# Performance work log

Hardware: AMD Instinct MI355X
Metric: run time of the kernel (lower is better)

## Reference

```python
import jax, jax.numpy as jnp
import numpy as np

NEG_SLOPE = 0.2

def gat_conv(x, edge, W, att_src, att_dst, bias, heads, out_ch, concat):
    # x: [N, F_in], edge: [2, E] (self-loops already included)
    N = x.shape[0]
    src, dst = edge[0], edge[1]
    h = (x @ W).reshape(N, heads, out_ch)                     # [N, H, C]
    a_src = jnp.sum(h * att_src, axis=-1)                     # [N, H]
    a_dst = jnp.sum(h * att_dst, axis=-1)                     # [N, H]
    e = jax.nn.leaky_relu(a_src[src] + a_dst[dst], NEG_SLOPE)  # [E, H]
    # segment softmax over incoming edges of each dst node
    e_max = jax.ops.segment_max(e, dst, num_segments=N)       # [N, H]
    e_exp = jnp.exp(e - e_max[dst])                           # [E, H]
    denom = jax.ops.segment_sum(e_exp, dst, num_segments=N)   # [N, H]
    alpha = e_exp / denom[dst]                                # [E, H]
    msg = h[src] * alpha[:, :, None]                          # [E, H, C]
    out = jax.ops.segment_sum(msg, dst, num_segments=N)       # [N, H, C]
    if concat:
        out = out.reshape(N, heads * out_ch)
    else:
        out = out.mean(axis=1)
    return out + bias


def setup_inputs() -> dict:
    key = jax.random.key(0)
    ks = jax.random.split(key, 10)
    N, E = 50000, 1600000
    F_in, H, C1, n_cls = 256, 4, 64, 40
    x = jax.random.normal(ks[0], (N, F_in), dtype=jnp.float32)
    edge_index = jax.random.randint(ks[1], (2, E), 0, N, dtype=jnp.int64)
    s1 = 1.0 / np.sqrt(F_in)
    s2 = 1.0 / np.sqrt(H * C1)
    return {
        "x": x,
        "edge_index": edge_index,
        "W1": jax.random.normal(ks[2], (F_in, H * C1), dtype=jnp.float32) * s1,
        "att_src1": jax.random.normal(ks[3], (H, C1), dtype=jnp.float32) * s2,
        "att_dst1": jax.random.normal(ks[4], (H, C1), dtype=jnp.float32) * s2,
        "b1": jnp.zeros((H * C1,), dtype=jnp.float32),
        "W2": jax.random.normal(ks[5], (H * C1, n_cls), dtype=jnp.float32) * s2,
        "att_src2": jax.random.normal(ks[6], (1, n_cls), dtype=jnp.float32) * 0.1,
        "att_dst2": jax.random.normal(ks[7], (1, n_cls), dtype=jnp.float32) * 0.1,
        "b2": jnp.zeros((n_cls,), dtype=jnp.float32),
    }


def reference(x, edge_index, W1, att_src1, att_dst1, b1, W2, att_src2, att_dst2, b2):
    N = x.shape[0]
    # PyG GATConv adds self-loops by default
    loops = jnp.arange(N, dtype=edge_index.dtype)
    edge = jnp.concatenate([edge_index, jnp.stack([loops, loops])], axis=1)
    # dropout is identity in eval mode
    h = gat_conv(x, edge, W1, att_src1, att_dst1, b1, heads=4, out_ch=64, concat=True)
    h = jax.nn.elu(h)
    out = gat_conv(h, edge, W2, att_src2, att_dst2, b2, heads=1, out_ch=40, concat=False)
    return out
```

## Files before the change

### kernel.cpp

```cpp
#include <hip/hip_runtime.h>
#include <hip/hip_bf16.h>

typedef short bf16x8 __attribute__((ext_vector_type(8)));
typedef float f32x4 __attribute__((ext_vector_type(4)));
typedef float f32x2 __attribute__((ext_vector_type(2)));
typedef unsigned short u16x8 __attribute__((ext_vector_type(8)));

#define CHUNK 4096
#define BCAP 16384

__device__ __forceinline__ float wred_sum(float v) {
  #pragma unroll
  for (int off = 32; off > 0; off >>= 1)
    v += __shfl_xor(v, off, 64);
  return v;
}
__device__ __forceinline__ float b2f(unsigned short u) {
  union { unsigned int i; float f; } x;
  x.i = ((unsigned int)u) << 16;
  return x.f;
}
__device__ __forceinline__ unsigned short f2bu(float f) {
  __hip_bfloat16 b = __float2bfloat16(f);
  return *(unsigned short*)&b;
}
__device__ __forceinline__ void pkfma(f32x2& acc, f32x2 v, f32x2 w) {
  asm volatile("v_pk_fma_f32 %0, %1, %2, %0" : "+v"(acc) : "v"(v), "v"(w));
}
__device__ __forceinline__ void qfma(f32x2* acc2, unsigned int u, f32x2 wp) {
  f32x2 a, b;
  a[0] = (float)(u & 0xFFu);         a[1] = (float)((u >> 8) & 0xFFu);
  b[0] = (float)((u >> 16) & 0xFFu); b[1] = (float)(u >> 24);
  pkfma(acc2[0], a, wp);
  pkfma(acc2[1], b, wp);
}
__device__ __forceinline__ void bffma(f32x2& acc, unsigned int up, f32x2 wp) {
  union { unsigned int i; float f; } lo, hi;
  lo.i = up << 16; hi.i = up & 0xFFFF0000u;
  f32x2 v; v[0] = lo.f; v[1] = hi.f;
  pkfma(acc, v, wp);
}
__device__ __forceinline__ float ldf(const void* p, long long i, int is16) {
  return is16 ? __bfloat162float(((const __hip_bfloat16*)p)[i])
              : ((const float*)p)[i];
}
__device__ __forceinline__ int edge_at(const int* e, long long idx, int is64) {
  return is64 ? (int)((const long long*)e)[idx] : e[idx];
}

__global__ void detect_kernel(const int* __restrict__ edge, int n_edge_check,
                              const unsigned int* __restrict__ xw, int n_x_check,
                              int* __restrict__ flag,
                              int* __restrict__ bcursor, int NB) {
  __shared__ int s_nz, s_cnt, s_tot;
  int tid = threadIdx.x;
  for (int b = tid; b < NB; b += 256) bcursor[b] = b * BCAP;
  if (tid == 0) { s_nz = 0; s_cnt = 0; s_tot = 0; }
  __syncthreads();
  int nz = 0;
  for (int k = tid; k < n_edge_check; k += 256)
    if (edge[2 * k + 1] != 0) nz = 1;
  if (nz) atomicOr(&s_nz, 1);
  int c = 0, t = 0;
  for (int k = tid; k < n_x_check; k += 256) {
    unsigned int w = xw[k];
    if (w == 0u) continue;
    t++;
    unsigned int e = (w >> 7) & 0xFFu;
    if (e >= 100u && e <= 150u) c++;
  }
  atomicAdd(&s_cnt, c);
  atomicAdd(&s_tot, t);
  __syncthreads();
  if (tid == 0) {
    flag[0] = (s_nz == 0) ? 1 : 0;
    flag[1] = (s_cnt * 10 > s_tot * 6) ? 1 : 0;
  }
}

__global__ __launch_bounds__(256) void partition_kernel(
    const int* __restrict__ edge, int E, int N, const int* __restrict__ flag,
    int* __restrict__ bcursor, unsigned int* __restrict__ part, int NB) {
  __shared__ int cnt[1024];
  __shared__ int loff[1025];
  __shared__ int gpos[1024];
  __shared__ int lcur[1024];
  __shared__ unsigned int staged[CHUNK];
  __shared__ int staged_addr[CHUNK];
  __shared__ int s[256];
  __shared__ int rbase;
  int tid = threadIdx.x;
  long long base = (long long)blockIdx.x * CHUNK;
  long long total = (long long)E + N;
  int maxa = NB * BCAP - 1;
  int here = (int)min((long long)CHUNK, total - base);
  for (int b = tid; b < NB; b += 256) cnt[b] = 0;
  if (tid == 0) rbase = 0;
  __syncthreads();
  int is64 = flag[0];
  int myb[16];
  unsigned int myp[16];
  #pragma unroll
  for (int j = 0; j < 16; j++) {
    long long i = base + j * 256 + tid;
    myb[j] = -1;
    if (i < total) {
      int d, sv;
      if (i < E) {
        sv = edge_at(edge, i, is64);
        d = edge_at(edge, (long long)E + i, is64);
      } else {
        sv = d = (int)(i - E);
      }
      d = min(max(d, 0), N - 1);
      sv = min(max(sv, 0), N - 1);
      myb[j] = d >> 8;
      myp[j] = ((unsigned int)(d & 255) << 24) | (unsigned int)sv;
      atomicAdd(&cnt[myb[j]], 1);
    }
  }
  __syncthreads();
  for (int c0 = 0; c0 < NB; c0 += 256) {
    int idx = c0 + tid;
    int v = (idx < NB) ? cnt[idx] : 0;
    s[tid] = v;
    __syncthreads();
    for (int off = 1; off < 256; off <<= 1) {
      int t = (tid >= off) ? s[tid - off] : 0;
      __syncthreads();
      s[tid] += t;
      __syncthreads();
    }
    int mb = rbase;
    if (idx < NB) loff[idx] = mb + s[tid] - v;
    __syncthreads();
    if (tid == 0) rbase = mb + s[255];
    __syncthreads();
  }
  __syncthreads();
  for (int b = tid; b < NB; b += 256) {
    int c = cnt[b];
    gpos[b] = c ? atomicAdd(&bcursor[b], c) : 0;
    lcur[b] = loff[b];
  }
  __syncthreads();
  #pragma unroll
  for (int j = 0; j < 16; j++) {
    if (myb[j] >= 0) {
      int b = myb[j];
      int slot = atomicAdd(&lcur[b], 1);
      staged[slot] = myp[j];
      staged_addr[slot] = min(gpos[b] + (slot - loff[b]), maxa);
    }
  }
  __syncthreads();
  for (int i = tid; i < here; i += 256)
    part[staged_addr[i]] = staged[i];
}

__global__ __launch_bounds__(256) void bucket_sort_kernel(
    const unsigned int* __restrict__ part, const int* __restrict__ bcursor,
    int N, int* __restrict__ indptr, int* __restrict__ iend,
    int* __restrict__ ssrc) {
  __shared__ int hist[256], cur[256];
  __shared__ int s[256];
  int tid = threadIdx.x;
  int b = blockIdx.x;
  int begin = b * BCAP, end = bcursor[b];
  hist[tid] = 0;
  __syncthreads();
  for (int i = begin + tid; i < end; i += 256)
    atomicAdd(&hist[part[i] >> 24], 1);
  __syncthreads();
  int v = hist[tid];
  s[tid] = v;
  __syncthreads();
  for (int off = 1; off < 256; off <<= 1) {
    int t = (tid >= off) ? s[tid - off] : 0;
    __syncthreads();
    s[tid] += t;
    __syncthreads();
  }
  int exc = s[tid] - v;
  cur[tid] = exc;
  int d = b * 256 + tid;
  if (d < N) { indptr[d] = begin + exc; iend[d] = begin + exc + v; }
  __syncthreads();
  for (int i = begin + tid; i < end; i += 256) {
    unsigned int p = part[i];
    int pos = begin + atomicAdd(&cur[p >> 24], 1);
    ssrc[pos] = (int)(p & 0xFFFFFFu);
  }
}

__global__ void prep_kernel(const void* __restrict__ x, __hip_bfloat16* __restrict__ xb,
                            long long n_valid4, long long nconv4,
                            const void* __restrict__ W1v, const void* __restrict__ W2v,
                            __hip_bfloat16* __restrict__ Wt1, __hip_bfloat16* __restrict__ Wt2,
                            int F, int HC, int C2, int C2p,
                            const int* __restrict__ dflag) {
  int f16 = dflag[1];
  long long i = blockIdx.x * 256LL + threadIdx.x;
  if (i < nconv4) {
    ushort4 o;
    if (i < n_valid4) {
      if (f16) {
        o = ((const ushort4*)x)[i];
      } else {
        float4 v = ((const float4*)x)[i];
        o.x = f2bu(v.x); o.y = f2bu(v.y); o.z = f2bu(v.z); o.w = f2bu(v.w);
      }
    } else {
      o.x = o.y = o.z = o.w = 0;
    }
    ((ushort4*)xb)[i] = o;
    return;
  }
  long long j = i - nconv4;
  int n1 = HC * F;
  if (j < n1) {
    int idx = (int)j;
    int n = idx / F, k = idx - n * F;
    Wt1[idx] = __float2bfloat16(ldf(W1v, (long long)k * HC + n, f16));
  } else {
    int jj = (int)(j - n1);
    if (jj >= C2p * HC) return;
    int n = jj / HC, k = jj - n * HC;
    float v = (n < C2) ? ldf(W2v, (long long)k * C2 + n, f16) : 0.f;
    Wt2[jj] = __float2bfloat16(v);
  }
}

__global__ __launch_bounds__(256) void mfma_gemm_kernel(
    const __hip_bfloat16* __restrict__ A, const __hip_bfloat16* __restrict__ BtT,
    __hip_bfloat16* __restrict__ Cb,
    const void* __restrict__ attS, const void* __restrict__ attD,
    float* __restrict__ aS, float* __restrict__ aD,
    float2* __restrict__ aSq, int att_stride,
    int M, int Nout, int K, int quant,
    unsigned char* __restrict__ h1q,
    const int* __restrict__ dflag) {
  int f16 = dflag[1];
  int tid = threadIdx.x;
  int w = tid >> 6, l = tid & 63;
  int m_lane = l & 15, q = l >> 4;
  int row0 = blockIdx.x * 64, col0 = blockIdx.y * 64;
  const __hip_bfloat16* Arow = A + (long long)(row0 + w * 16 + m_lane) * K + q * 8;
  const __hip_bfloat16* Brow = BtT + (long long)(col0 + m_lane) * K + q * 8;
  f32x4 acc[4] = {};
  #pragma unroll 4
  for (int k0 = 0; k0 < K; k0 += 32) {
    bf16x8 af = *(const bf16x8*)(Arow + k0);
    #pragma unroll
    for (int t = 0; t < 4; t++) {
      bf16x8 bf = *(const bf16x8*)(Brow + (long long)t * 16 * K + k0);
      acc[t] = __builtin_amdgcn_mfma_f32_16x16x32_bf16(af, bf, acc[t], 0, 0, 0);
    }
  }
  #pragma unroll
  for (int r = 0; r < 4; r++) {
    int gr = row0 + w * 16 + q * 4 + r;
    float ps = 0.f, pd = 0.f, vmax = 0.f;
    #pragma unroll
    for (int t = 0; t < 4; t++) {
      int gc = col0 + t * 16 + m_lane;
      float v = acc[t][r];
      if (gc < Nout) {
        ps += v * ldf(attS, gc, f16);
        pd += v * ldf(attD, gc, f16);
        vmax = fmaxf(vmax, fabsf(v));
        if (!quant && gr < M) Cb[(long long)gr * Nout + gc] = __float2bfloat16(v);
      }
    }
    #pragma unroll
    for (int off = 1; off < 16; off <<= 1) {
      ps += __shfl_xor(ps, off, 64);
      pd += __shfl_xor(pd, off, 64);
      vmax = fmaxf(vmax, __shfl_xor(vmax, off, 64));
    }
    if (quant && gr < M) {
      float qinv = (vmax > 0.f) ? 127.f / vmax : 0.f;
      #pragma unroll
      for (int t = 0; t < 4; t++) {
        int gc = col0 + t * 16 + m_lane;
        h1q[(long long)gr * 256 + gc] =
            (unsigned char)(__float2int_rn(acc[t][r] * qinv) + 128);
      }
      if (m_lane == 0) {
        float2 sq; sq.x = ps; sq.y = vmax * (1.f / 127.f);
        aSq[(long long)gr * att_stride + blockIdx.y] = sq;
      }
    }
    if (m_lane == 0 && gr < M) {
      if (!quant) aS[(long long)gr * att_stride + blockIdx.y] = ps;
      aD[(long long)gr * att_stride + blockIdx.y] = pd;
    }
  }
}

__global__ __launch_bounds__(256) void aggregate1_kernel(
    const int* __restrict__ indptr, const int* __restrict__ iend,
    const int* __restrict__ ssrc,
    const unsigned char* __restrict__ h1q, const float2* __restrict__ a_sq,
    const float* __restrict__ a_dst, const void* __restrict__ b1,
    __hip_bfloat16* __restrict__ h2b, int N, const int* __restrict__ dflag) {
  int f16 = dflag[1];
  int w = threadIdx.x >> 6, l = threadIdx.x & 63;
  int d = blockIdx.x * 4 + w;
  if (d >= N) return;
  int q = l >> 4;
  int e16 = l & 15;
  int hb = (l & 12) << 2;
  int chb = (l & 15) << 4;
  int begin = indptr[d], end = iend[d];
  float adst = a_dst[d * 4 + q];
  int s0 = ssrc[begin];
  float den = 0.f, accS = 0.f;
  f32x2 acc2[8] = {};
  for (int c = begin; c < end; c += 32) {
    int cnt = end - c;
    int sj0 = s0, sj1 = s0;
    float wj0 = 0.f, wj1 = 0.f, ws0 = 0.f, ws1 = 0.f;
    if (e16 < cnt) {
      sj0 = ssrc[c + e16];
      float2 t = a_sq[sj0 * 4 + q];
      float e = t.x + adst;
      e = (e > 0.f) ? e : 0.2f * e;
      wj0 = __expf(e);
      ws0 = wj0 * t.y;
    }
    if (e16 + 16 < cnt) {
      sj1 = ssrc[c + e16 + 16];
      float2 t = a_sq[sj1 * 4 + q];
      float e = t.x + adst;
      e = (e > 0.f) ? e : 0.2f * e;
      wj1 = __expf(e);
      ws1 = wj1 * t.y;
    }
    den += wj0 + wj1;
    int m0 = cnt < 16 ? cnt : 16;
    int m1 = cnt - 16; m1 = m1 < 0 ? 0 : (m1 > 16 ? 16 : m1);
    int j0 = (m0 + 3) >> 2, j1 = (m1 + 3) >> 2;
    #pragma unroll 4
    for (int j = 0; j < j0; j++) {
      int idx = hb + 4 * j + q;
      int s = __shfl(sj0, idx, 64);
      float wt = __shfl(ws0, idx, 64);
      accS += wt;
      f32x2 wp; wp[0] = wt; wp[1] = wt;
      uint4 uv = *(const uint4*)(h1q + (long long)s * 256 + chb);
      qfma(&acc2[0], uv.x, wp);
      qfma(&acc2[2], uv.y, wp);
      qfma(&acc2[4], uv.z, wp);
      qfma(&acc2[6], uv.w, wp);
    }
    #pragma unroll 4
    for (int j = 0; j < j1; j++) {
      int idx = hb + 4 * j + q;
      int s = __shfl(sj1, idx, 64);
      float wt = __shfl(ws1, idx, 64);
      accS += wt;
      f32x2 wp; wp[0] = wt; wp[1] = wt;
      uint4 uv = *(const uint4*)(h1q + (long long)s * 256 + chb);
      qfma(&acc2[0], uv.x, wp);
      qfma(&acc2[2], uv.y, wp);
      qfma(&acc2[4], uv.z, wp);
      qfma(&acc2[6], uv.w, wp);
    }
  }
  float* af = (float*)acc2;
  #pragma unroll
  for (int i = 0; i < 16; i++) {
    af[i] += __shfl_xor(af[i], 16, 64);
    af[i] += __shfl_xor(af[i], 32, 64);
  }
  accS += __shfl_xor(accS, 16, 64);
  accS += __shfl_xor(accS, 32, 64);
  #pragma unroll
  for (int off = 1; off < 16; off <<= 1)
    den += __shfl_xor(den, off, 64);
  float deh = __shfl(den, hb, 64);
  float inv = 1.f / deh;
  if (l < 16) {
    u16x8 o0, o1;
    #pragma unroll
    for (int i = 0; i < 16; i++) {
      float v = (af[i] - 128.f * accS) * inv + ldf(b1, chb + i, f16);
      v = (v > 0.f) ? v : (__expf(v) - 1.f);
      if (i < 8) o0[i] = f2bu(v); else o1[i - 8] = f2bu(v);
    }
    u16x8* dst = (u16x8*)((unsigned short*)h2b + (long long)d * 256 + chb);
    dst[0] = o0;
    dst[1] = o1;
  }
}

__global__ __launch_bounds__(256) void aggregate2_kernel(
    const int* __restrict__ indptr, const int* __restrict__ iend,
    const int* __restrict__ ssrc,
    const __hip_bfloat16* __restrict__ gb, const float* __restrict__ a_src,
    const float* __restrict__ a_dst, const void* __restrict__ b2,
    void* __restrict__ out, int N, int C, const int* __restrict__ dflag) {
  int f16 = dflag[1];
  int w = threadIdx.x >> 6, l = threadIdx.x & 63;
  int d = blockIdx.x * 4 + w;
  if (d >= N) return;
  int begin = indptr[d], end = iend[d];
  float adst = a_dst[d];
  int eg = l / 10;
  int cq = l - eg * 10;
  bool act = (eg < 6);
  int s0 = ssrc[begin];
  float den = 0.f;
  f32x2 acc01 = {0.f, 0.f}, acc23 = {0.f, 0.f};
  for (int c = begin; c < end; c += 64) {
    int cnt = min(64, end - c);
    int sj = s0;
    float wj = 0.f;
    if (l < cnt) {
      sj = ssrc[c + l];
      float e = a_src[sj] + adst;
      e = (e > 0.f) ? e : 0.2f * e;
      wj = __expf(e);
    }
    den += wj;
    int jm = (cnt + 5) / 6;
    #pragma unroll 4
    for (int j = 0; j < jm; j++) {
      int idx = 6 * j + eg;
      int s = __shfl(sj, idx & 63, 64);
      float wt = __shfl(wj, idx & 63, 64);
      if (!act || idx >= cnt) wt = 0.f;
      uint2 gv = *(const uint2*)((const unsigned short*)gb +
                                 (long long)s * C + 4 * cq);
      f32x2 wp; wp[0] = wt; wp[1] = wt;
      bffma(acc01, gv.x, wp);
      bffma(acc23, gv.y, wp);
    }
  }
  den = wred_sum(den);
  float inv = 1.f / den;
  float a0 = acc01[0], a1 = acc01[1], a2 = acc23[0], a3 = acc23[1];
  #pragma unroll
  for (int k = 1; k < 6; k++) {
    int srcl = cq + 10 * k;
    a0 += __shfl(acc01[0], srcl, 64);
    a1 += __shfl(acc01[1], srcl, 64);
    a2 += __shfl(acc23[0], srcl, 64);
    a3 += __shfl(acc23[1], srcl, 64);
  }
  if (l < 10) {
    float v0 = a0 * inv + ldf(b2, 4 * l + 0, f16);
    float v1 = a1 * inv + ldf(b2, 4 * l + 1, f16);
    float v2 = a2 * inv + ldf(b2, 4 * l + 2, f16);
    float v3 = a3 * inv + ldf(b2, 4 * l + 3, f16);
    long long o = (long long)d * C + 4 * l;
    if (f16) {
      ushort4 ov;
      ov.x = f2bu(v0); ov.y = f2bu(v1); ov.z = f2bu(v2); ov.w = f2bu(v3);
      *(ushort4*)((unsigned short*)out + o) = ov;
    } else {
      float4 ov;
      ov.x = v0; ov.y = v1; ov.z = v2; ov.w = v3;
      *(float4*)((float*)out + o) = ov;
    }
  }
}

extern "C" void kernel_launch(void* const* d_in, const int* in_sizes, int n_in,
                              void* d_out, int out_size, void* d_ws, size_t ws_size,
                              hipStream_t stream) {
  const void* x   = d_in[0];
  const int* edge = (const int*)d_in[1];
  const void* W1  = d_in[2];
  const void* as1 = d_in[3];
  const void* ad1 = d_in[4];
  const void* b1  = d_in[5];
  const void* W2  = d_in[6];
  const void* as2 = d_in[7];
  const void* ad2 = d_in[8];
  const void* b2  = d_in[9];

  const int F  = 256;
  const int HC = 256;
  const int N  = in_sizes[0] / F;
  const int E  = in_sizes[1] / 2;
  const int C2 = in_sizes[9];
  const int C2p = 64;
  const int total = E + N;
  const int NB = (N + 255) / 256;
  const int Mpad = ((N + 63) / 64) * 64;

  char* p = (char*)d_ws;
  auto alloc = [&](size_t bytes) -> void* {
    void* r = (void*)p;
    p += (bytes + 255) & ~(size_t)255;
    return r;
  };
  __hip_bfloat16* xb  = (__hip_bfloat16*)alloc((size_t)Mpad * F * 2);
  unsigned char*  h1q = (unsigned char*)alloc((size_t)Mpad * HC);
  __hip_bfloat16* h2b = (__hip_bfloat16*)alloc((size_t)Mpad * HC * 2);
  __hip_bfloat16* gb  = (__hip_bfloat16*)alloc((size_t)Mpad * C2 * 2);
  __hip_bfloat16* Wt1 = (__hip_bfloat16*)alloc((size_t)HC * F * 2);
  __hip_bfloat16* Wt2 = (__hip_bfloat16*)alloc((size_t)C2p * HC * 2);
  float2* a_sq1 = (float2*)alloc((size_t)N * 4 * 8);
  float* a_dst1 = (float*)alloc((size_t)N * 4 * 4);
  float* a_src2 = (float*)alloc((size_t)N * 4);
  float* a_dst2 = (float*)alloc((size_t)N * 4);
  unsigned int* part = (unsigned int*)alloc((size_t)NB * BCAP * 4);
  int* ssrc     = (int*)alloc((size_t)NB * BCAP * 4);
  int* bcursor  = (int*)alloc((size_t)NB * 4);
  int* indptr   = (int*)alloc((size_t)(N + 1) * 4);
  int* iend     = (int*)alloc((size_t)N * 4);
  int* flag     = (int*)alloc(256);

  detect_kernel<<<1, 256, 0, stream>>>(edge, E < 2048 ? E : 2048,
                                       (const unsigned int*)x, 4096, flag,
                                       bcursor, NB);
  int nch = (total + CHUNK - 1) / CHUNK;
  partition_kernel<<<nch, 256, 0, stream>>>(edge, E, N, flag, bcursor, part, NB);
  bucket_sort_kernel<<<NB, 256, 0, stream>>>(part, bcursor, N, indptr, iend, ssrc);

  long long nconv4 = (long long)Mpad * F / 4;
  long long nprep = nconv4 + (long long)HC * F + (long long)C2p * HC;
  prep_kernel<<<(int)((nprep + 255) / 256), 256, 0, stream>>>(
      x, xb, (long long)N * F / 4, nconv4, W1, W2, Wt1, Wt2, F, HC, C2, C2p, flag);

  dim3 g1(Mpad / 64, HC / 64);
  mfma_gemm_kernel<<<g1, 256, 0, stream>>>(xb, Wt1, nullptr,
                                           as1, ad1, nullptr, a_dst1, a_sq1, 4,
                                           N, HC, F, 1, h1q, flag);
  aggregate1_kernel<<<(N + 3) / 4, 256, 0, stream>>>(indptr, iend, ssrc, h1q, a_sq1,
                                                     a_dst1, b1, h2b, N, flag);

  dim3 g2(Mpad / 64, 1);
  mfma_gemm_kernel<<<g2, 256, 0, stream>>>(h2b, Wt2, gb,
                                           as2, ad2, a_src2, a_dst2, nullptr, 1,
                                           N, C2, HC, 0, nullptr, flag);
  aggregate2_kernel<<<(N + 3) / 4, 256, 0, stream>>>(indptr, iend, ssrc, gb, a_src2, a_dst2,
                                                     b2, d_out, N, C2, flag);
}
```

Baseline: 375.8 us.

## Use grid-stride persistent aggregation and widen edge chunks to 48

Both aggregation kernels now launch a fixed 2048-block grid, and each wave loops over destination nodes with a grid stride instead of handling one node per wave. Aggregate1 processes edges in chunks of 48 (three 16-edge groups) with the three gathers interleaved in one loop, which puts more independent loads in flight. The asm volatile on the packed FMA is dropped so the compiler can schedule it more freely. The aim is less block launch overhead and more memory-level parallelism; the cost is a possible load imbalance across waves from the fixed grid and higher register use.

```diff
diff --git a/kernel.cpp b/kernel.cpp
--- a/kernel.cpp
+++ b/kernel.cpp
@@ -25,7 +25,7 @@
   return *(unsigned short*)&b;
 }
 __device__ __forceinline__ void pkfma(f32x2& acc, f32x2 v, f32x2 w) {
-  asm volatile("v_pk_fma_f32 %0, %1, %2, %0" : "+v"(acc) : "v"(v), "v"(w));
+  asm("v_pk_fma_f32 %0, %1, %2, %0" : "+v"(acc) : "v"(v), "v"(w));
 }
 __device__ __forceinline__ void qfma(f32x2* acc2, unsigned int u, f32x2 wp) {
   f32x2 a, b;
@@ -306,92 +306,112 @@
     __hip_bfloat16* __restrict__ h2b, int N, const int* __restrict__ dflag) {
   int f16 = dflag[1];
   int w = threadIdx.x >> 6, l = threadIdx.x & 63;
-  int d = blockIdx.x * 4 + w;
-  if (d >= N) return;
   int q = l >> 4;
   int e16 = l & 15;
   int hb = (l & 12) << 2;
   int chb = (l & 15) << 4;
-  int begin = indptr[d], end = iend[d];
-  float adst = a_dst[d * 4 + q];
-  int s0 = ssrc[begin];
-  float den = 0.f, accS = 0.f;
-  f32x2 acc2[8] = {};
-  for (int c = begin; c < end; c += 32) {
-    int cnt = end - c;
-    int sj0 = s0, sj1 = s0;
-    float wj0 = 0.f, wj1 = 0.f, ws0 = 0.f, ws1 = 0.f;
-    if (e16 < cnt) {
-      sj0 = ssrc[c + e16];
-      float2 t = a_sq[sj0 * 4 + q];
-      float e = t.x + adst;
-      e = (e > 0.f) ? e : 0.2f * e;
-      wj0 = __expf(e);
-      ws0 = wj0 * t.y;
-    }
-    if (e16 + 16 < cnt) {
-      sj1 = ssrc[c + e16 + 16];
-      float2 t = a_sq[sj1 * 4 + q];
-      float e = t.x + adst;
-      e = (e > 0.f) ? e : 0.2f * e;
-      wj1 = __expf(e);
-      ws1 = wj1 * t.y;
-    }
-    den += wj0 + wj1;
-    int m0 = cnt < 16 ? cnt : 16;
-    int m1 = cnt - 16; m1 = m1 < 0 ? 0 : (m1 > 16 ? 16 : m1);
-    int j0 = (m0 + 3) >> 2, j1 = (m1 + 3) >> 2;
-    #pragma unroll 4
-    for (int j = 0; j < j0; j++) {
-      int idx = hb + 4 * j + q;
-      int s = __shfl(sj0, idx, 64);
-      float wt = __shfl(ws0, idx, 64);
-      accS += wt;
-      f32x2 wp; wp[0] = wt; wp[1] = wt;
-      uint4 uv = *(const uint4*)(h1q + (long long)s * 256 + chb);
-      qfma(&acc2[0], uv.x, wp);
-      qfma(&acc2[2], uv.y, wp);
-      qfma(&acc2[4], uv.z, wp);
-      qfma(&acc2[6], uv.w, wp);
-    }
-    #pragma unroll 4
-    for (int j = 0; j < j1; j++) {
-      int idx = hb + 4 * j + q;
-      int s = __shfl(sj1, idx, 64);
-      float wt = __shfl(ws1, idx, 64);
-      accS += wt;
-      f32x2 wp; wp[0] = wt; wp[1] = wt;
-      uint4 uv = *(const uint4*)(h1q + (long long)s * 256 + chb);
-      qfma(&acc2[0], uv.x, wp);
-      qfma(&acc2[2], uv.y, wp);
-      qfma(&acc2[4], uv.z, wp);
-      qfma(&acc2[6], uv.w, wp);
-    }
-  }
-  float* af = (float*)acc2;
-  #pragma unroll
-  for (int i = 0; i < 16; i++) {
-    af[i] += __shfl_xor(af[i], 16, 64);
-    af[i] += __shfl_xor(af[i], 32, 64);
-  }
-  accS += __shfl_xor(accS, 16, 64);
-  accS += __shfl_xor(accS, 32, 64);
-  #pragma unroll
-  for (int off = 1; off < 16; off <<= 1)
-    den += __shfl_xor(den, off, 64);
-  float deh = __shfl(den, hb, 64);
-  float inv = 1.f / deh;
-  if (l < 16) {
-    u16x8 o0, o1;
+  int stride = gridDim.x * 4;
+  for (int d = blockIdx.x * 4 + w; d < N; d += stride) {
+    int begin = indptr[d], end = iend[d];
+    float adst = a_dst[d * 4 + q];
+    int s0 = ssrc[begin];
+    float den = 0.f, accS = 0.f;
+    f32x2 acc2[8] = {};
+    for (int c = begin; c < end; c += 48) {
+      int cnt = end - c;
+      int sj0 = s0, sj1 = s0, sj2 = s0;
+      float ws0 = 0.f, ws1 = 0.f, ws2 = 0.f;
+      if (e16 < cnt) {
+        sj0 = ssrc[c + e16];
+        float2 t = a_sq[sj0 * 4 + q];
+        float e = t.x + adst;
+        e = (e > 0.f) ? e : 0.2f * e;
+        float wj = __expf(e);
+        den += wj; ws0 = wj * t.y;
+      }
+      if (e16 + 16 < cnt) {
+        sj1 = ssrc[c + 16 + e16];
+        float2 t = a_sq[sj1 * 4 + q];
+        float e = t.x + adst;
+        e = (e > 0.f) ? e : 0.2f * e;
+        float wj = __expf(e);
+        den += wj; ws1 = wj * t.y;
+      }
+      if (e16 + 32 < cnt) {
+        sj2 = ssrc[c + 32 + e16];
+        float2 t = a_sq[sj2 * 4 + q];
+        float e = t.x + adst;
+        e = (e > 0.f) ? e : 0.2f * e;
+        float wj = __expf(e);
+        den += wj; ws2 = wj * t.y;
+      }
+      int m0 = cnt < 16 ? cnt : 16;
+      int m1 = cnt - 16; m1 = m1 < 0 ? 0 : (m1 > 16 ? 16 : m1);
+      int m2 = cnt - 32; m2 = m2 < 0 ? 0 : (m2 > 16 ? 16 : m2);
+      int j0 = (m0 + 3) >> 2, j1 = (m1 + 3) >> 2, j2 = (m2 + 3) >> 2;
+      #pragma unroll 4
+      for (int j = 0; j < j0; j++) {
+        int idx = hb + 4 * j + q;
+        {
+          int s = __shfl(sj0, idx, 64);
+          float wt = __shfl(ws0, idx, 64);
+          accS += wt;
+          f32x2 wp; wp[0] = wt; wp[1] = wt;
+          uint4 uv = *(const uint4*)(h1q + (long long)s * 256 + chb);
+          qfma(&acc2[0], uv.x, wp);
+          qfma(&acc2[2], uv.y, wp);
+          qfma(&acc2[4], uv.z, wp);
+          qfma(&acc2[6], uv.w, wp);
+        }
+        if (j < j1) {
+          int s = __shfl(sj1, idx, 64);
+          float wt = __shfl(ws1, idx, 64);
+          accS += wt;
+          f32x2 wp; wp[0] = wt; wp[1] = wt;
+          uint4 uv = *(const uint4*)(h1q + (long long)s * 256 + chb);
+          qfma(&acc2[0], uv.x, wp);
+          qfma(&acc2[2], uv.y, wp);
+          qfma(&acc2[4], uv.z, wp);
+          qfma(&acc2[6], uv.w, wp);
+        }
+        if (j < j2) {
+          int s = __shfl(sj2, idx, 64);
+          float wt = __shfl(ws2, idx, 64);
+          accS += wt;
+          f32x2 wp; wp[0] = wt; wp[1] = wt;
+          uint4 uv = *(const uint4*)(h1q + (long long)s * 256 + chb);
+          qfma(&acc2[0], uv.x, wp);
+          qfma(&acc2[2], uv.y, wp);
+          qfma(&acc2[4], uv.z, wp);
+          qfma(&acc2[6], uv.w, wp);
+        }
+      }
+    }
+    float* af = (float*)acc2;
     #pragma unroll
     for (int i = 0; i < 16; i++) {
-      float v = (af[i] - 128.f * accS) * inv + ldf(b1, chb + i, f16);
-      v = (v > 0.f) ? v : (__expf(v) - 1.f);
-      if (i < 8) o0[i] = f2bu(v); else o1[i - 8] = f2bu(v);
-    }
-    u16x8* dst = (u16x8*)((unsigned short*)h2b + (long long)d * 256 + chb);
-    dst[0] = o0;
-    dst[1] = o1;
+      af[i] += __shfl_xor(af[i], 16, 64);
+      af[i] += __shfl_xor(af[i], 32, 64);
+    }
+    accS += __shfl_xor(accS, 16, 64);
+    accS += __shfl_xor(accS, 32, 64);
+    #pragma unroll
+    for (int off = 1; off < 16; off <<= 1)
+      den += __shfl_xor(den, off, 64);
+    float deh = __shfl(den, hb, 64);
+    float inv = 1.f / deh;
+    if (l < 16) {
+      u16x8 o0, o1;
+      #pragma unroll
+      for (int i = 0; i < 16; i++) {
+        float v = (af[i] - 128.f * accS) * inv + ldf(b1, chb + i, f16);
+        v = (v > 0.f) ? v : (__expf(v) - 1.f);
+        if (i < 8) o0[i] = f2bu(v); else o1[i - 8] = f2bu(v);
+      }
+      u16x8* dst = (u16x8*)((unsigned short*)h2b + (long long)d * 256 + chb);
+      dst[0] = o0;
+      dst[1] = o1;
+    }
   }
 }
 
@@ -403,66 +423,67 @@
     void* __restrict__ out, int N, int C, const int* __restrict__ dflag) {
   int f16 = dflag[1];
   int w = threadIdx.x >> 6, l = threadIdx.x & 63;
-  int d = blockIdx.x * 4 + w;
-  if (d >= N) return;
-  int begin = indptr[d], end = iend[d];
-  float adst = a_dst[d];
   int eg = l / 10;
   int cq = l - eg * 10;
   bool act = (eg < 6);
-  int s0 = ssrc[begin];
-  float den = 0.f;
-  f32x2 acc01 = {0.f, 0.f}, acc23 = {0.f, 0.f};
-  for (int c = begin; c < end; c += 64) {
-    int cnt = min(64, end - c);
-    int sj = s0;
-    float wj = 0.f;
-    if (l < cnt) {
-      sj = ssrc[c + l];
-      float e = a_src[sj] + adst;
-      e = (e > 0.f) ? e : 0.2f * e;
-      wj = __expf(e);
-    }
-    den += wj;
-    int jm = (cnt + 5) / 6;
-    #pragma unroll 4
-    for (int j = 0; j < jm; j++) {
-      int idx = 6 * j + eg;
-      int s = __shfl(sj, idx & 63, 64);
-      float wt = __shfl(wj, idx & 63, 64);
-      if (!act || idx >= cnt) wt = 0.f;
-      uint2 gv = *(const uint2*)((const unsigned short*)gb +
-                                 (long long)s * C + 4 * cq);
-      f32x2 wp; wp[0] = wt; wp[1] = wt;
-      bffma(acc01, gv.x, wp);
-      bffma(acc23, gv.y, wp);
-    }
-  }
-  den = wred_sum(den);
-  float inv = 1.f / den;
-  float a0 = acc01[0], a1 = acc01[1], a2 = acc23[0], a3 = acc23[1];
-  #pragma unroll
-  for (int k = 1; k < 6; k++) {
-    int srcl = cq + 10 * k;
-    a0 += __shfl(acc01[0], srcl, 64);
-    a1 += __shfl(acc01[1], srcl, 64);
-    a2 += __shfl(acc23[0], srcl, 64);
-    a3 += __shfl(acc23[1], srcl, 64);
-  }
-  if (l < 10) {
-    float v0 = a0 * inv + ldf(b2, 4 * l + 0, f16);
-    float v1 = a1 * inv + ldf(b2, 4 * l + 1, f16);
-    float v2 = a2 * inv + ldf(b2, 4 * l + 2, f16);
-    float v3 = a3 * inv + ldf(b2, 4 * l + 3, f16);
-    long long o = (long long)d * C + 4 * l;
-    if (f16) {
-      ushort4 ov;
-      ov.x = f2bu(v0); ov.y = f2bu(v1); ov.z = f2bu(v2); ov.w = f2bu(v3);
-      *(ushort4*)((unsigned short*)out + o) = ov;
-    } else {
-      float4 ov;
-      ov.x = v0; ov.y = v1; ov.z = v2; ov.w = v3;
-      *(float4*)((float*)out + o) = ov;
+  int stride = gridDim.x * 4;
+  for (int d = blockIdx.x * 4 + w; d < N; d += stride) {
+    int begin = indptr[d], end = iend[d];
+    float adst = a_dst[d];
+    int s0 = ssrc[begin];
+    float den = 0.f;
+    f32x2 acc01 = {0.f, 0.f}, acc23 = {0.f, 0.f};
+    for (int c = begin; c < end; c += 64) {
+      int cnt = min(64, end - c);
+      int sj = s0;
+      float wj = 0.f;
+      if (l < cnt) {
+        sj = ssrc[c + l];
+        float e = a_src[sj] + adst;
+        e = (e > 0.f) ? e : 0.2f * e;
+        wj = __expf(e);
+      }
+      den += wj;
+      int jm = (cnt + 5) / 6;
+      #pragma unroll 4
+      for (int j = 0; j < jm; j++) {
+        int idx = 6 * j + eg;
+        int s = __shfl(sj, idx & 63, 64);
+        float wt = __shfl(wj, idx & 63, 64);
+        if (!act || idx >= cnt) wt = 0.f;
+        uint2 gv = *(const uint2*)((const unsigned short*)gb +
+                                   (long long)s * C + 4 * cq);
+        f32x2 wp; wp[0] = wt; wp[1] = wt;
+        bffma(acc01, gv.x, wp);
+        bffma(acc23, gv.y, wp);
+      }
+    }
+    den = wred_sum(den);
+    float inv = 1.f / den;
+    float a0 = acc01[0], a1 = acc01[1], a2 = acc23[0], a3 = acc23[1];
+    #pragma unroll
+    for (int k = 1; k < 6; k++) {
+      int srcl = cq + 10 * k;
+      a0 += __shfl(acc01[0], srcl, 64);
+      a1 += __shfl(acc01[1], srcl, 64);
+      a2 += __shfl(acc23[0], srcl, 64);
+      a3 += __shfl(acc23[1], srcl, 64);
+    }
+    if (l < 10) {
+      float v0 = a0 * inv + ldf(b2, 4 * l + 0, f16);
+      float v1 = a1 * inv + ldf(b2, 4 * l + 1, f16);
+      float v2 = a2 * inv + ldf(b2, 4 * l + 2, f16);
+      float v3 = a3 * inv + ldf(b2, 4 * l + 3, f16);
+      long long o = (long long)d * C + 4 * l;
+      if (f16) {
+        ushort4 ov;
+        ov.x = f2bu(v0); ov.y = f2bu(v1); ov.z = f2bu(v2); ov.w = f2bu(v3);
+        *(ushort4*)((unsigned short*)out + o) = ov;
+      } else {
+        float4 ov;
+        ov.x = v0; ov.y = v1; ov.z = v2; ov.w = v3;
+        *(float4*)((float*)out + o) = ov;
+      }
     }
   }
 }
@@ -530,13 +551,13 @@
   mfma_gemm_kernel<<<g1, 256, 0, stream>>>(xb, Wt1, nullptr,
                                            as1, ad1, nullptr, a_dst1, a_sq1, 4,
                                            N, HC, F, 1, h1q, flag);
-  aggregate1_kernel<<<(N + 3) / 4, 256, 0, stream>>>(indptr, iend, ssrc, h1q, a_sq1,
-                                                     a_dst1, b1, h2b, N, flag);
+  aggregate1_kernel<<<2048, 256, 0, stream>>>(indptr, iend, ssrc, h1q, a_sq1,
+                                              a_dst1, b1, h2b, N, flag);
 
   dim3 g2(Mpad / 64, 1);
   mfma_gemm_kernel<<<g2, 256, 0, stream>>>(h2b, Wt2, gb,
                                            as2, ad2, a_src2, a_dst2, nullptr, 1,
                                            N, C2, HC, 0, nullptr, flag);
-  aggregate2_kernel<<<(N + 3) / 4, 256, 0, stream>>>(indptr, iend, ssrc, gb, a_src2, a_dst2,
-                                                     b2, d_out, N, C2, flag);
-}
+  aggregate2_kernel<<<2048, 256, 0, stream>>>(indptr, iend, ssrc, gb, a_src2, a_dst2,
+                                              b2, d_out, N, C2, flag);
+}
```

Measured after the change: 399.5 us. +6.3%, slower.

## Compute all heads per GEMM block and process four nodes per wave in aggregation

Applied to the files above, without the earlier changes.

The first GEMM becomes a template that computes all 256 output columns (16 MFMA tiles) in one block, so each A row is read once instead of four times. The attention vectors are preloaded into registers. Both aggregation kernels now loop over four destination nodes per wavefront, which cuts the grid to a quarter, and the two edge-half loops in aggregate1 are interleaved for more memory-level parallelism. The inline asm loses its volatile qualifier so the compiler may schedule it. The trade-off is higher register pressure from 16 accumulators and fewer GEMM blocks, plus more load imbalance from serialized per-node work.

```diff
diff --git a/kernel.cpp b/kernel.cpp
--- a/kernel.cpp
+++ b/kernel.cpp
@@ -25,7 +25,7 @@
   return *(unsigned short*)&b;
 }
 __device__ __forceinline__ void pkfma(f32x2& acc, f32x2 v, f32x2 w) {
-  asm volatile("v_pk_fma_f32 %0, %1, %2, %0" : "+v"(acc) : "v"(v), "v"(w));
+  asm("v_pk_fma_f32 %0, %1, %2, %0" : "+v"(acc) : "v"(v), "v"(w));
 }
 __device__ __forceinline__ void qfma(f32x2* acc2, unsigned int u, f32x2 wp) {
   f32x2 a, b;
@@ -231,28 +231,36 @@
   }
 }
 
+template<int NT, int NH>
 __global__ __launch_bounds__(256) void mfma_gemm_kernel(
     const __hip_bfloat16* __restrict__ A, const __hip_bfloat16* __restrict__ BtT,
     __hip_bfloat16* __restrict__ Cb,
     const void* __restrict__ attS, const void* __restrict__ attD,
     float* __restrict__ aS, float* __restrict__ aD,
-    float2* __restrict__ aSq, int att_stride,
+    float2* __restrict__ aSq,
     int M, int Nout, int K, int quant,
     unsigned char* __restrict__ h1q,
     const int* __restrict__ dflag) {
+  constexpr int TPH = NT / NH;
   int f16 = dflag[1];
   int tid = threadIdx.x;
   int w = tid >> 6, l = tid & 63;
   int m_lane = l & 15, q = l >> 4;
-  int row0 = blockIdx.x * 64, col0 = blockIdx.y * 64;
+  int row0 = blockIdx.x * 64;
   const __hip_bfloat16* Arow = A + (long long)(row0 + w * 16 + m_lane) * K + q * 8;
-  const __hip_bfloat16* Brow = BtT + (long long)(col0 + m_lane) * K + q * 8;
-  f32x4 acc[4] = {};
-  #pragma unroll 4
+  const __hip_bfloat16* Brow = BtT + (long long)m_lane * K + q * 8;
+  float attS_v[NT], attD_v[NT];
+  #pragma unroll
+  for (int t = 0; t < NT; t++) {
+    int gc = t * 16 + m_lane;
+    attS_v[t] = (gc < Nout) ? ldf(attS, gc, f16) : 0.f;
+    attD_v[t] = (gc < Nout) ? ldf(attD, gc, f16) : 0.f;
+  }
+  f32x4 acc[NT] = {};
   for (int k0 = 0; k0 < K; k0 += 32) {
     bf16x8 af = *(const bf16x8*)(Arow + k0);
     #pragma unroll
-    for (int t = 0; t < 4; t++) {
+    for (int t = 0; t < NT; t++) {
       bf16x8 bf = *(const bf16x8*)(Brow + (long long)t * 16 * K + k0);
       acc[t] = __builtin_amdgcn_mfma_f32_16x16x32_bf16(af, bf, acc[t], 0, 0, 0);
     }
@@ -260,40 +268,46 @@
   #pragma unroll
   for (int r = 0; r < 4; r++) {
     int gr = row0 + w * 16 + q * 4 + r;
-    float ps = 0.f, pd = 0.f, vmax = 0.f;
+    bool rowok = (gr < M);
     #pragma unroll
-    for (int t = 0; t < 4; t++) {
-      int gc = col0 + t * 16 + m_lane;
-      float v = acc[t][r];
-      if (gc < Nout) {
-        ps += v * ldf(attS, gc, f16);
-        pd += v * ldf(attD, gc, f16);
-        vmax = fmaxf(vmax, fabsf(v));
-        if (!quant && gr < M) Cb[(long long)gr * Nout + gc] = __float2bfloat16(v);
-      }
-    }
-    #pragma unroll
-    for (int off = 1; off < 16; off <<= 1) {
-      ps += __shfl_xor(ps, off, 64);
-      pd += __shfl_xor(pd, off, 64);
-      vmax = fmaxf(vmax, __shfl_xor(vmax, off, 64));
-    }
-    if (quant && gr < M) {
-      float qinv = (vmax > 0.f) ? 127.f / vmax : 0.f;
+    for (int h = 0; h < NH; h++) {
+      float ps = 0.f, pd = 0.f, vmax = 0.f;
       #pragma unroll
-      for (int t = 0; t < 4; t++) {
-        int gc = col0 + t * 16 + m_lane;
-        h1q[(long long)gr * 256 + gc] =
-            (unsigned char)(__float2int_rn(acc[t][r] * qinv) + 128);
-      }
-      if (m_lane == 0) {
-        float2 sq; sq.x = ps; sq.y = vmax * (1.f / 127.f);
-        aSq[(long long)gr * att_stride + blockIdx.y] = sq;
-      }
-    }
-    if (m_lane == 0 && gr < M) {
-      if (!quant) aS[(long long)gr * att_stride + blockIdx.y] = ps;
-      aD[(long long)gr * att_stride + blockIdx.y] = pd;
+      for (int tt = 0; tt < TPH; tt++) {
+        int t = h * TPH + tt;
+        int gc = t * 16 + m_lane;
+        float v = acc[t][r];
+        if (gc < Nout) {
+          ps += v * attS_v[t];
+          pd += v * attD_v[t];
+          vmax = fmaxf(vmax, fabsf(v));
+          if (!quant && rowok) Cb[(long long)gr * Nout + gc] = __float2bfloat16(v);
+        }
+      }
+      #pragma unroll
+      for (int off = 1; off < 16; off <<= 1) {
+        ps += __shfl_xor(ps, off, 64);
+        pd += __shfl_xor(pd, off, 64);
+        vmax = fmaxf(vmax, __shfl_xor(vmax, off, 64));
+      }
+      if (quant && rowok) {
+        float qinv = (vmax > 0.f) ? 127.f / vmax : 0.f;
+        #pragma unroll
+        for (int tt = 0; tt < TPH; tt++) {
+          int t = h * TPH + tt;
+          int gc = t * 16 + m_lane;
+          h1q[(long long)gr * 256 + gc] =
+              (unsigned char)(__float2int_rn(acc[t][r] * qinv) + 128);
+        }
+        if (m_lane == 0) {
+          float2 sq; sq.x = ps; sq.y = vmax * (1.f / 127.f);
+          aSq[(long long)gr * NH + h] = sq;
+        }
+      }
+      if (m_lane == 0 && rowok) {
+        if (!quant) aS[(long long)gr * NH + h] = ps;
+        aD[(long long)gr * NH + h] = pd;
+      }
     }
   }
 }
@@ -306,92 +320,95 @@
     __hip_bfloat16* __restrict__ h2b, int N, const int* __restrict__ dflag) {
   int f16 = dflag[1];
   int w = threadIdx.x >> 6, l = threadIdx.x & 63;
-  int d = blockIdx.x * 4 + w;
-  if (d >= N) return;
   int q = l >> 4;
   int e16 = l & 15;
   int hb = (l & 12) << 2;
   int chb = (l & 15) << 4;
-  int begin = indptr[d], end = iend[d];
-  float adst = a_dst[d * 4 + q];
-  int s0 = ssrc[begin];
-  float den = 0.f, accS = 0.f;
-  f32x2 acc2[8] = {};
-  for (int c = begin; c < end; c += 32) {
-    int cnt = end - c;
-    int sj0 = s0, sj1 = s0;
-    float wj0 = 0.f, wj1 = 0.f, ws0 = 0.f, ws1 = 0.f;
-    if (e16 < cnt) {
-      sj0 = ssrc[c + e16];
-      float2 t = a_sq[sj0 * 4 + q];
-      float e = t.x + adst;
-      e = (e > 0.f) ? e : 0.2f * e;
-      wj0 = __expf(e);
-      ws0 = wj0 * t.y;
-    }
-    if (e16 + 16 < cnt) {
-      sj1 = ssrc[c + e16 + 16];
-      float2 t = a_sq[sj1 * 4 + q];
-      float e = t.x + adst;
-      e = (e > 0.f) ? e : 0.2f * e;
-      wj1 = __expf(e);
-      ws1 = wj1 * t.y;
-    }
-    den += wj0 + wj1;
-    int m0 = cnt < 16 ? cnt : 16;
-    int m1 = cnt - 16; m1 = m1 < 0 ? 0 : (m1 > 16 ? 16 : m1);
-    int j0 = (m0 + 3) >> 2, j1 = (m1 + 3) >> 2;
-    #pragma unroll 4
-    for (int j = 0; j < j0; j++) {
-      int idx = hb + 4 * j + q;
-      int s = __shfl(sj0, idx, 64);
-      float wt = __shfl(ws0, idx, 64);
-      accS += wt;
-      f32x2 wp; wp[0] = wt; wp[1] = wt;
-      uint4 uv = *(const uint4*)(h1q + (long long)s * 256 + chb);
-      qfma(&acc2[0], uv.x, wp);
-      qfma(&acc2[2], uv.y, wp);
-      qfma(&acc2[4], uv.z, wp);
-      qfma(&acc2[6], uv.w, wp);
-    }
-    #pragma unroll 4
-    for (int j = 0; j < j1; j++) {
-      int idx = hb + 4 * j + q;
-      int s = __shfl(sj1, idx, 64);
-      float wt = __shfl(ws1, idx, 64);
-      accS += wt;
-      f32x2 wp; wp[0] = wt; wp[1] = wt;
-      uint4 uv = *(const uint4*)(h1q + (long long)s * 256 + chb);
-      qfma(&acc2[0], uv.x, wp);
-      qfma(&acc2[2], uv.y, wp);
-      qfma(&acc2[4], uv.z, wp);
-      qfma(&acc2[6], uv.w, wp);
-    }
-  }
-  float* af = (float*)acc2;
-  #pragma unroll
-  for (int i = 0; i < 16; i++) {
-    af[i] += __shfl_xor(af[i], 16, 64);
-    af[i] += __shfl_xor(af[i], 32, 64);
-  }
-  accS += __shfl_xor(accS, 16, 64);
-  accS += __shfl_xor(accS, 32, 64);
-  #pragma unroll
-  for (int off = 1; off < 16; off <<= 1)
-    den += __shfl_xor(den, off, 64);
-  float deh = __shfl(den, hb, 64);
-  float inv = 1.f / deh;
-  if (l < 16) {
-    u16x8 o0, o1;
+  int d0 = (blockIdx.x * 4 + w) * 4;
+  #pragma unroll 1
+  for (int dd = 0; dd < 4; dd++) {
+    int d = d0 + dd;
+    if (d >= N) break;
+    int begin = indptr[d], end = iend[d];
+    float adst = a_dst[d * 4 + q];
+    int s0 = ssrc[begin];
+    float den = 0.f, accS = 0.f;
+    f32x2 acc2[8] = {};
+    for (int c = begin; c < end; c += 32) {
+      int cnt = end - c;
+      int sj0 = s0, sj1 = s0;
+      float ws0 = 0.f, ws1 = 0.f;
+      if (e16 < cnt) {
+        sj0 = ssrc[c + e16];
+        float2 t = a_sq[sj0 * 4 + q];
+        float e = t.x + adst;
+        e = (e > 0.f) ? e : 0.2f * e;
+        float wj = __expf(e);
+        den += wj; ws0 = wj * t.y;
+      }
+      if (e16 + 16 < cnt) {
+        sj1 = ssrc[c + 16 + e16];
+        float2 t = a_sq[sj1 * 4 + q];
+        float e = t.x + adst;
+        e = (e > 0.f) ? e : 0.2f * e;
+        float wj = __expf(e);
+        den += wj; ws1 = wj * t.y;
+      }
+      int m0 = cnt < 16 ? cnt : 16;
+      int m1 = cnt - 16; m1 = m1 < 0 ? 0 : (m1 > 16 ? 16 : m1);
+      int j0 = (m0 + 3) >> 2, j1 = (m1 + 3) >> 2;
+      #pragma unroll 4
+      for (int j = 0; j < j0; j++) {
+        int idx = hb + 4 * j + q;
+        {
+          int s = __shfl(sj0, idx, 64);
+          float wt = __shfl(ws0, idx, 64);
+          accS += wt;
+          f32x2 wp; wp[0] = wt; wp[1] = wt;
+          uint4 uv = *(const uint4*)(h1q + (long long)s * 256 + chb);
+          qfma(&acc2[0], uv.x, wp);
+          qfma(&acc2[2], uv.y, wp);
+          qfma(&acc2[4], uv.z, wp);
+          qfma(&acc2[6], uv.w, wp);
+        }
+        if (j < j1) {
+          int s = __shfl(sj1, idx, 64);
+          float wt = __shfl(ws1, idx, 64);
+          accS += wt;
+          f32x2 wp; wp[0] = wt; wp[1] = wt;
+          uint4 uv = *(const uint4*)(h1q + (long long)s * 256 + chb);
+          qfma(&acc2[0], uv.x, wp);
+          qfma(&acc2[2], uv.y, wp);
+          qfma(&acc2[4], uv.z, wp);
+          qfma(&acc2[6], uv.w, wp);
+        }
+      }
+    }
+    float* af = (float*)acc2;
     #pragma unroll
     for (int i = 0; i < 16; i++) {
-      float v = (af[i] - 128.f * accS) * inv + ldf(b1, chb + i, f16);
-      v = (v > 0.f) ? v : (__expf(v) - 1.f);
-      if (i < 8) o0[i] = f2bu(v); else o1[i - 8] = f2bu(v);
-    }
-    u16x8* dst = (u16x8*)((unsigned short*)h2b + (long long)d * 256 + chb);
-    dst[0] = o0;
-    dst[1] = o1;
+      af[i] += __shfl_xor(af[i], 16, 64);
+      af[i] += __shfl_xor(af[i], 32, 64);
+    }
+    accS += __shfl_xor(accS, 16, 64);
+    accS += __shfl_xor(accS, 32, 64);
+    #pragma unroll
+    for (int off = 1; off < 16; off <<= 1)
+      den += __shfl_xor(den, off, 64);
+    float deh = __shfl(den, hb, 64);
+    float inv = 1.f / deh;
+    if (l < 16) {
+      u16x8 o0, o1;
+      #pragma unroll
+      for (int i = 0; i < 16; i++) {
+        float v = (af[i] - 128.f * accS) * inv + ldf(b1, chb + i, f16);
+        v = (v > 0.f) ? v : (__expf(v) - 1.f);
+        if (i < 8) o0[i] = f2bu(v); else o1[i - 8] = f2bu(v);
+      }
+      u16x8* dst = (u16x8*)((unsigned short*)h2b + (long long)d * 256 + chb);
+      dst[0] = o0;
+      dst[1] = o1;
+    }
   }
 }
 
@@ -403,66 +420,70 @@
     void* __restrict__ out, int N, int C, const int* __restrict__ dflag) {
   int f16 = dflag[1];
   int w = threadIdx.x >> 6, l = threadIdx.x & 63;
-  int d = blockIdx.x * 4 + w;
-  if (d >= N) return;
-  int begin = indptr[d], end = iend[d];
-  float adst = a_dst[d];
   int eg = l / 10;
   int cq = l - eg * 10;
   bool act = (eg < 6);
-  int s0 = ssrc[begin];
-  float den = 0.f;
-  f32x2 acc01 = {0.f, 0.f}, acc23 = {0.f, 0.f};
-  for (int c = begin; c < end; c += 64) {
-    int cnt = min(64, end - c);
-    int sj = s0;
-    float wj = 0.f;
-    if (l < cnt) {
-      sj = ssrc[c + l];
-      float e = a_src[sj] + adst;
-      e = (e > 0.f) ? e : 0.2f * e;
-      wj = __expf(e);
-    }
-    den += wj;
-    int jm = (cnt + 5) / 6;
-    #pragma unroll 4
-    for (int j = 0; j < jm; j++) {
-      int idx = 6 * j + eg;
-      int s = __shfl(sj, idx & 63, 64);
-      float wt = __shfl(wj, idx & 63, 64);
-      if (!act || idx >= cnt) wt = 0.f;
-      uint2 gv = *(const uint2*)((const unsigned short*)gb +
-                                 (long long)s * C + 4 * cq);
-      f32x2 wp; wp[0] = wt; wp[1] = wt;
-      bffma(acc01, gv.x, wp);
-      bffma(acc23, gv.y, wp);
-    }
-  }
-  den = wred_sum(den);
-  float inv = 1.f / den;
-  float a0 = acc01[0], a1 = acc01[1], a2 = acc23[0], a3 = acc23[1];
-  #pragma unroll
-  for (int k = 1; k < 6; k++) {
-    int srcl = cq + 10 * k;
-    a0 += __shfl(acc01[0], srcl, 64);
-    a1 += __shfl(acc01[1], srcl, 64);
-    a2 += __shfl(acc23[0], srcl, 64);
-    a3 += __shfl(acc23[1], srcl, 64);
-  }
-  if (l < 10) {
-    float v0 = a0 * inv + ldf(b2, 4 * l + 0, f16);
-    float v1 = a1 * inv + ldf(b2, 4 * l + 1, f16);
-    float v2 = a2 * inv + ldf(b2, 4 * l + 2, f16);
-    float v3 = a3 * inv + ldf(b2, 4 * l + 3, f16);
-    long long o = (long long)d * C + 4 * l;
-    if (f16) {
-      ushort4 ov;
-      ov.x = f2bu(v0); ov.y = f2bu(v1); ov.z = f2bu(v2); ov.w = f2bu(v3);
-      *(ushort4*)((unsigned short*)out + o) = ov;
-    } else {
-      float4 ov;
-      ov.x = v0; ov.y = v1; ov.z = v2; ov.w = v3;
-      *(float4*)((float*)out + o) = ov;
+  int d0 = (blockIdx.x * 4 + w) * 4;
+  #pragma unroll 1
+  for (int dd = 0; dd < 4; dd++) {
+    int d = d0 + dd;
+    if (d >= N) break;
+    int begin = indptr[d], end = iend[d];
+    float adst = a_dst[d];
+    int s0 = ssrc[begin];
+    float den = 0.f;
+    f32x2 acc01 = {0.f, 0.f}, acc23 = {0.f, 0.f};
+    for (int c = begin; c < end; c += 64) {
+      int cnt = min(64, end - c);
+      int sj = s0;
+      float wj = 0.f;
+      if (l < cnt) {
+        sj = ssrc[c + l];
+        float e = a_src[sj] + adst;
+        e = (e > 0.f) ? e : 0.2f * e;
+        wj = __expf(e);
+      }
+      den += wj;
+      int jm = (cnt + 5) / 6;
+      #pragma unroll 4
+      for (int j = 0; j < jm; j++) {
+        int idx = 6 * j + eg;
+        int s = __shfl(sj, idx & 63, 64);
+        float wt = __shfl(wj, idx & 63, 64);
+        if (!act || idx >= cnt) wt = 0.f;
+        uint2 gv = *(const uint2*)((const unsigned short*)gb +
+                                   (long long)s * C + 4 * cq);
+        f32x2 wp; wp[0] = wt; wp[1] = wt;
+        bffma(acc01, gv.x, wp);
+        bffma(acc23, gv.y, wp);
+      }
+    }
+    den = wred_sum(den);
+    float inv = 1.f / den;
+    float a0 = acc01[0], a1 = acc01[1], a2 = acc23[0], a3 = acc23[1];
+    #pragma unroll
+    for (int k = 1; k < 6; k++) {
+      int srcl = cq + 10 * k;
+      a0 += __shfl(acc01[0], srcl, 64);
+      a1 += __shfl(acc01[1], srcl, 64);
+      a2 += __shfl(acc23[0], srcl, 64);
+      a3 += __shfl(acc23[1], srcl, 64);
+    }
+    if (l < 10) {
+      float v0 = a0 * inv + ldf(b2, 4 * l + 0, f16);
+      float v1 = a1 * inv + ldf(b2, 4 * l + 1, f16);
+      float v2 = a2 * inv + ldf(b2, 4 * l + 2, f16);
+      float v3 = a3 * inv + ldf(b2, 4 * l + 3, f16);
+      long long o = (long long)d * C + 4 * l;
+      if (f16) {
+        ushort4 ov;
+        ov.x = f2bu(v0); ov.y = f2bu(v1); ov.z = f2bu(v2); ov.w = f2bu(v3);
+        *(ushort4*)((unsigned short*)out + o) = ov;
+      } else {
+        float4 ov;
+        ov.x = v0; ov.y = v1; ov.z = v2; ov.w = v3;
+        *(float4*)((float*)out + o) = ov;
+      }
     }
   }
 }
@@ -526,17 +547,15 @@
   prep_kernel<<<(int)((nprep + 255) / 256), 256, 0, stream>>>(
       x, xb, (long long)N * F / 4, nconv4, W1, W2, Wt1, Wt2, F, HC, C2, C2p, flag);
 
-  dim3 g1(Mpad / 64, HC / 64);
-  mfma_gemm_kernel<<<g1, 256, 0, stream>>>(xb, Wt1, nullptr,
-                                           as1, ad1, nullptr, a_dst1, a_sq1, 4,
-                                           N, HC, F, 1, h1q, flag);
-  aggregate1_kernel<<<(N + 3) / 4, 256, 0, stream>>>(indptr, iend, ssrc, h1q, a_sq1,
-                                                     a_dst1, b1, h2b, N, flag);
-
-  dim3 g2(Mpad / 64, 1);
-  mfma_gemm_kernel<<<g2, 256, 0, stream>>>(h2b, Wt2, gb,
-                                           as2, ad2, a_src2, a_dst2, nullptr, 1,
-                                           N, C2, HC, 0, nullptr, flag);
-  aggregate2_kernel<<<(N + 3) / 4, 256, 0, stream>>>(indptr, iend, ssrc, gb, a_src2, a_dst2,
-                                                     b2, d_out, N, C2, flag);
-}
+  mfma_gemm_kernel<16, 4><<<Mpad / 64, 256, 0, stream>>>(
+      xb, Wt1, nullptr, as1, ad1, nullptr, a_dst1, a_sq1,
+      N, HC, F, 1, h1q, flag);
+  aggregate1_kernel<<<(N + 15) / 16, 256, 0, stream>>>(indptr, iend, ssrc, h1q, a_sq1,
+                                                       a_dst1, b1, h2b, N, flag);
+
+  mfma_gemm_kernel<4, 1><<<Mpad / 64, 256, 0, stream>>>(
+      h2b, Wt2, gb, as2, ad2, a_src2, a_dst2, nullptr,
+      N, C2, HC, 0, nullptr, flag);
+  aggregate2_kernel<<<(N + 15) / 16, 256, 0, stream>>>(indptr, iend, ssrc, gb, a_src2, a_dst2,
+                                                       b2, d_out, N, C2, flag);
+}
```

Result: slower. 410.5 us (+9.2%).
